# Performance work log

Measured on AMD Instinct MI355X. Metric: run time of the kernel, lower is better.

## Reference

```python
import jax, jax.numpy as jnp
import numpy as np

IN_DIM = 768
N_HEADS = 12
HEAD_DIM = IN_DIM // N_HEADS


def setup_inputs() -> dict:
    key = jax.random.key(0)
    k1, k2, k3, k4, k5 = jax.random.split(key, 5)
    x = jax.random.normal(k1, (2, 2048, IN_DIM), dtype=jnp.float32)
    s = 1.0 / np.sqrt(IN_DIM)
    W_qkv = jax.random.uniform(k2, (IN_DIM, 3 * IN_DIM), jnp.float32, -s, s)
    b_qkv = jax.random.uniform(k3, (3 * IN_DIM,), jnp.float32, -s, s)
    W_out = jax.random.uniform(k4, (IN_DIM, IN_DIM), jnp.float32, -s, s)
    b_out = jax.random.uniform(k5, (IN_DIM,), jnp.float32, -s, s)
    return {"x": x, "W_qkv": W_qkv, "b_qkv": b_qkv, "W_out": W_out, "b_out": b_out}


def reference(x, W_qkv, b_qkv, W_out, b_out):
    B, N, D = x.shape
    qkv = x @ W_qkv + b_qkv  # [B, N, 3D]
    qkv = qkv.reshape(B, N, 3, N_HEADS, HEAD_DIM)
    qkv = jnp.transpose(qkv, (2, 0, 3, 1, 4))  # [3, B, H, N, Dh]
    q, k, v = qkv[0], qkv[1], qkv[2]
    scale = 1.0 / np.sqrt(HEAD_DIM)
    scores = jnp.einsum("bhqd,bhkd->bhqk", q, k) * scale  # [B, H, N, N]
    attn = jax.nn.softmax(scores, axis=-1)
    out = jnp.einsum("bhqk,bhkd->bhqd", attn, v)  # [B, H, N, Dh]
    out = jnp.transpose(out, (0, 2, 1, 3)).reshape(B, N, D)
    return out @ W_out + b_out
```

## Files before the change

### kernel.cpp

```cpp
#include <hip/hip_runtime.h>

#define DEVI __device__ __forceinline__

typedef __attribute__((ext_vector_type(8))) short short8;
typedef __attribute__((ext_vector_type(4))) float f32x4;

DEVI unsigned short f32_to_bf16(float f) {
  unsigned int u = __float_as_uint(f);
  u += 0x7fffu + ((u >> 16) & 1u);
  return (unsigned short)(u >> 16);
}
DEVI float bf16_to_f32(unsigned short h) {
  return __uint_as_float(((unsigned int)h) << 16);
}

DEVI void gld_lds16(const void* g, void* l) {
  __builtin_amdgcn_global_load_lds(
      (__attribute__((address_space(1))) void*)(g),
      (__attribute__((address_space(3))) void*)(l), 16, 0, 0);
}

__global__ void k_cast_bf16(const float* __restrict__ in, unsigned short* __restrict__ out,
                            int total8) {
  int i = blockIdx.x * blockDim.x + threadIdx.x;
  if (i >= total8) return;
  const float* src = in + i * 8;
  short8 v;
#pragma unroll
  for (int j = 0; j < 8; ++j) v[j] = (short)f32_to_bf16(src[j]);
  *(short8*)&out[(size_t)i * 8] = v;
}

__global__ __launch_bounds__(256) void k_cast_Bt(const float* __restrict__ W,
                                                 unsigned short* __restrict__ Wt,
                                                 int K, int N) {
  int kt = blockIdx.x, nt = blockIdx.y;
  __shared__ float t[32][33];
  int tid = threadIdx.x;
#pragma unroll
  for (int p = 0; p < 4; ++p) {
    int idx = tid + p * 256;
    int rr = idx >> 5, cc = idx & 31;
    t[rr][cc] = W[(size_t)(kt * 32 + rr) * N + nt * 32 + cc];
  }
  __syncthreads();
#pragma unroll
  for (int p = 0; p < 4; ++p) {
    int idx = tid + p * 256;
    int rn = idx >> 5, ck = idx & 31;
    Wt[(size_t)(nt * 32 + rn) * K + kt * 32 + ck] = f32_to_bf16(t[ck][rn]);
  }
}

__global__ __launch_bounds__(256) void k_gemm_qkv(const unsigned short* __restrict__ A,
                                                  const unsigned short* __restrict__ Bt,
                                                  const float* __restrict__ bias,
                                                  int M, int N, int K,
                                                  unsigned short* __restrict__ Qo,
                                                  unsigned short* __restrict__ Ko,
                                                  unsigned short* __restrict__ Vo) {
  __shared__ __align__(16) unsigned short As[128 * 32];
  __shared__ __align__(16) unsigned short Bs[128 * 32];
  int tid = threadIdx.x;
  int tm = blockIdx.x, tn = blockIdx.y;
  int lane = tid & 63, wid = tid >> 6;
  int wr = wid >> 1, wc = wid & 1;
  int g = lane >> 4, lr = lane & 15;
  f32x4 acc[4][4] = {};
  int srow = tid >> 2;
  int scol = (tid & 3) * 8;
  const unsigned short* Ab = A + (size_t)tm * 128 * K;
  const unsigned short* Bb = Bt + (size_t)tn * 128 * K;
  for (int k0 = 0; k0 < K; k0 += 32) {
    gld_lds16(Ab + (size_t)srow * K + k0 + scol, &As[srow * 32 + scol]);
    gld_lds16(Ab + (size_t)(srow + 64) * K + k0 + scol, &As[(srow + 64) * 32 + scol]);
    gld_lds16(Bb + (size_t)srow * K + k0 + scol, &Bs[srow * 32 + scol]);
    gld_lds16(Bb + (size_t)(srow + 64) * K + k0 + scol, &Bs[(srow + 64) * 32 + scol]);
    __syncthreads();
    short8 a[4], b[4];
#pragma unroll
    for (int m = 0; m < 4; ++m)
      a[m] = *(const short8*)&As[(wr * 64 + m * 16 + lr) * 32 + g * 8];
#pragma unroll
    for (int n = 0; n < 4; ++n)
      b[n] = *(const short8*)&Bs[(wc * 64 + n * 16 + lr) * 32 + g * 8];
#pragma unroll
    for (int m = 0; m < 4; ++m)
#pragma unroll
      for (int n = 0; n < 4; ++n)
        acc[m][n] = __builtin_amdgcn_mfma_f32_16x16x32_bf16(a[m], b[n], acc[m][n], 0, 0, 0);
    __syncthreads();
  }
  const float QSCALE = 0.125f * 1.4426950408889634f;
#pragma unroll
  for (int m = 0; m < 4; ++m) {
#pragma unroll
    for (int n = 0; n < 4; ++n) {
      int col = tn * 128 + wc * 64 + n * 16 + lr;
      float bv = bias[col];
      int sec = (col >= 1536) ? 2 : ((col >= 768) ? 1 : 0);
      int c = col - sec * 768;
      int hh = c >> 6, d = c & 63;
#pragma unroll
      for (int j = 0; j < 4; ++j) {
        int row = tm * 128 + wr * 64 + m * 16 + g * 4 + j;
        int bb = row >> 11, nn = row & 2047;
        size_t dst = (((size_t)(bb * 12 + hh) << 11) + nn) * 64 + d;
        float outv = acc[m][n][j] + bv;
        if (sec == 0) {
          Qo[dst] = f32_to_bf16(outv * QSCALE);
        } else if (sec == 1) {
          Ko[dst] = f32_to_bf16(outv);
        } else {
          Vo[dst] = f32_to_bf16(outv);
        }
      }
    }
  }
}

__global__ __launch_bounds__(256) void k_gemm2(const unsigned short* __restrict__ A,
                                               const unsigned short* __restrict__ Bt,
                                               const float* __restrict__ bias,
                                               float* __restrict__ C,
                                               int M, int N, int K) {
  __shared__ __align__(16) unsigned short As[64 * 32];
  __shared__ __align__(16) unsigned short Bs[64 * 32];
  int tid = threadIdx.x;
  int tm = blockIdx.x, tn = blockIdx.y;
  int lane = tid & 63, wid = tid >> 6;
  int wr = wid >> 1, wc = wid & 1;
  int g = lane >> 4, lr = lane & 15;
  f32x4 acc[2][2] = {};
  int srow = tid >> 2;
  int scol = (tid & 3) * 8;
  const unsigned short* Ab = A + (size_t)tm * 64 * K;
  const unsigned short* Bb = Bt + (size_t)tn * 64 * K;
  for (int k0 = 0; k0 < K; k0 += 32) {
    gld_lds16(Ab + (size_t)srow * K + k0 + scol, &As[srow * 32 + scol]);
    gld_lds16(Bb + (size_t)srow * K + k0 + scol, &Bs[srow * 32 + scol]);
    __syncthreads();
    short8 a[2], b[2];
#pragma unroll
    for (int m = 0; m < 2; ++m)
      a[m] = *(const short8*)&As[(wr * 32 + m * 16 + lr) * 32 + g * 8];
#pragma unroll
    for (int n = 0; n < 2; ++n)
      b[n] = *(const short8*)&Bs[(wc * 32 + n * 16 + lr) * 32 + g * 8];
#pragma unroll
    for (int m = 0; m < 2; ++m)
#pragma unroll
      for (int n = 0; n < 2; ++n)
        acc[m][n] = __builtin_amdgcn_mfma_f32_16x16x32_bf16(a[m], b[n], acc[m][n], 0, 0, 0);
    __syncthreads();
  }
#pragma unroll
  for (int m = 0; m < 2; ++m) {
#pragma unroll
    for (int n = 0; n < 2; ++n) {
      int col = tn * 64 + wc * 32 + n * 16 + lr;
      float bv = bias[col];
#pragma unroll
      for (int j = 0; j < 4; ++j) {
        int row = tm * 64 + wr * 32 + m * 16 + g * 4 + j;
        C[(size_t)row * N + col] = acc[m][n][j] + bv;
      }
    }
  }
}

__global__ __launch_bounds__(256) void k_v_transpose(const unsigned short* __restrict__ Vc,
                                                     unsigned short* __restrict__ Vt) {
  int bh = blockIdx.x;
  int nt = blockIdx.y;
  __shared__ unsigned short s[64][65];
  int tid = threadIdx.x;
  int r = tid >> 2;
#pragma unroll
  for (int p = 0; p < 2; ++p) {
    int c = (tid & 3) + p * 4;
    short8 v = *(const short8*)&Vc[((size_t)(bh * 2048 + nt * 64 + r)) * 64 + c * 8];
#pragma unroll
    for (int ii = 0; ii < 8; ++ii) s[r][c * 8 + ii] = (unsigned short)v[ii];
  }
  __syncthreads();
  int d = tid >> 2;
#pragma unroll
  for (int p = 0; p < 2; ++p) {
    int c = (tid & 3) + p * 4;
    short8 w;
#pragma unroll
    for (int ii = 0; ii < 8; ++ii) w[ii] = (short)s[c * 8 + ii][d];
    *(short8*)&Vt[((size_t)bh * 64 + d) * 2048 + nt * 64 + c * 8] = w;
  }
}


#define ATTN_STAGE(KSB, VSB, T)                                                          \
  {                                                                                      \
    int kv0 = (T) * 64;                                                                  \
    _Pragma("unroll") for (int it = 0; it < 2; ++it) {                                   \
      int L = tid + it * 256;                                                            \
      int rw = L >> 3, s7 = L & 7;                                                       \
      gld_lds16(Kb + (size_t)(khead + kv0 + rw) * 64 + ((s7 ^ (rw & 7)) * 8),            \
                &KSB[L * 8]);                                                            \
      gld_lds16(Vt + (size_t)(vhead + rw) * 2048 + kv0 + ((s7 ^ (rw & 7)) * 8),          \
                &VSB[L * 8]);                                                            \
    }                                                                                    \
  }

#define PS_WRITE(M)                                                                      \
  {                                                                                      \
    unsigned int d0, d1;                                                                 \
    asm("v_cvt_pk_bf16_f32 %0, %1, %2" : "=v"(d0) : "v"(s[M][0]), "v"(s[M][1]));         \
    asm("v_cvt_pk_bf16_f32 %0, %1, %2" : "=v"(d1) : "v"(s[M][2]), "v"(s[M][3]));         \
    uint2 w;                                                                             \
    w.x = d0;                                                                            \
    w.y = d1;                                                                            \
    *(uint2*)&Ps[wid][lr * 64 + ((((M)*2 + (g >> 1)) ^ lr) & 7) * 8 + (g & 1) * 4] = w;  \
  }

#define PV_KK(KK, VSB)                                                                   \
  {                                                                                      \
    short8 pa = *(const short8*)&Ps[wid][lr * 64 + ((((KK)*4 + g) ^ lr) & 7) * 8];       \
    __builtin_amdgcn_s_setprio(1);                                                       \
    _Pragma("unroll") for (int nt = 0; nt < 4; ++nt) {                                   \
      short8 vb = *(const short8*)&VSB[(nt * 16 + lr) * 64 +                             \
                                       ((((KK)*4 + g) ^ (lr & 7)) & 7) * 8];             \
      oacc[nt] = __builtin_amdgcn_mfma_f32_16x16x32_bf16(pa, vb, oacc[nt], 0, 0, 0);     \
    }                                                                                    \
    __builtin_amdgcn_s_setprio(0);                                                       \
  }

#define PROC_TILE(KSB, VSB)                                                              \
  {                                                                                      \
    f32x4 s[4];                                                                          \
    __builtin_amdgcn_s_setprio(1);                                                       \
    _Pragma("unroll") for (int m = 0; m < 4; ++m) {                                      \
      short8 kf0 = *(const short8*)&KSB[(m * 16 + lr) * 64 + ((g ^ (lr & 7)) * 8)];      \
      short8 kf1 =                                                                       \
          *(const short8*)&KSB[(m * 16 + lr) * 64 + (((g + 4) ^ (lr & 7)) * 8)];         \
      f32x4 z = {0.f, 0.f, 0.f, 0.f};                                                    \
      z = __builtin_amdgcn_mfma_f32_16x16x32_bf16(kf0, qf0, z, 0, 0, 0);                 \
      s[m] = __builtin_amdgcn_mfma_f32_16x16x32_bf16(kf1, qf1, z, 0, 0, 0);              \
    }                                                                                    \
    __builtin_amdgcn_s_setprio(0);                                                       \
    _Pragma("unroll") for (int m = 0; m < 4; ++m) {                                      \
      _Pragma("unroll") for (int j = 0; j < 4; ++j) {                                    \
        float pv = exp2f(s[m][j]);                                                       \
        s[m][j] = pv;                                                                    \
        lrun += pv;                                                                      \
      }                                                                                  \
    }                                                                                    \
    PS_WRITE(0)                                                                          \
    PS_WRITE(1)                                                                          \
    PV_KK(0, VSB)                                                                        \
    PS_WRITE(2)                                                                          \
    PS_WRITE(3)                                                                          \
    PV_KK(1, VSB)                                                                        \
  }

__global__ __launch_bounds__(256, 4) void k_attn(const unsigned short* __restrict__ Qb,
                                                 const unsigned short* __restrict__ Kb,
                                                 const unsigned short* __restrict__ Vt,
                                                 unsigned short* __restrict__ Xh) {
  int bh = blockIdx.x;
  int qb = blockIdx.y;
  int b = bh / 12, h = bh - b * 12;
  __shared__ __align__(16) unsigned short Ks0[64 * 64], Ks1[64 * 64];
  __shared__ __align__(16) unsigned short Vs0[64 * 64], Vs1[64 * 64];
  __shared__ __align__(16) unsigned short Ps[4][16 * 64];
  int tid = threadIdx.x;
  int wid = tid >> 6, lane = tid & 63;
  int g = lane >> 4, lr = lane & 15;
  int khead = bh * 2048;
  int vhead = bh * 64;
  int q0 = qb * 64 + wid * 16;

  short8 qf0 = *(const short8*)&Qb[(size_t)(khead + q0 + lr) * 64 + g * 8];
  short8 qf1 = *(const short8*)&Qb[(size_t)(khead + q0 + lr) * 64 + 32 + g * 8];

  float lrun = 0.f;
  f32x4 oacc[4] = {};

  ATTN_STAGE(Ks0, Vs0, 0);
  __syncthreads();
#pragma unroll 1
  for (int tt = 0; tt < 16; ++tt) {
    ATTN_STAGE(Ks1, Vs1, 2 * tt + 1);
    PROC_TILE(Ks0, Vs0);
    __syncthreads();
    if (tt < 15) ATTN_STAGE(Ks0, Vs0, 2 * tt + 2);
    PROC_TILE(Ks1, Vs1);
    __syncthreads();
  }

  lrun += __shfl_xor(lrun, 16, 64);
  lrun += __shfl_xor(lrun, 32, 64);
  float linv = 1.0f / lrun;
  float lf[4];
#pragma unroll
  for (int j = 0; j < 4; ++j) lf[j] = __shfl(linv, g * 4 + j, 64);
#pragma unroll
  for (int nt = 0; nt < 4; ++nt)
#pragma unroll
    for (int j = 0; j < 4; ++j) {
      int row = b * 2048 + q0 + g * 4 + j;
      int col = h * 64 + nt * 16 + lr;
      Xh[(size_t)row * 768 + col] = f32_to_bf16(oacc[nt][j] * lf[j]);
    }
}

extern "C" void kernel_launch(void* const* d_in, const int* in_sizes, int n_in,
                              void* d_out, int out_size, void* d_ws, size_t ws_size,
                              hipStream_t stream) {
  const float* x = (const float*)d_in[0];
  const float* W_qkv = (const float*)d_in[1];
  const float* b_qkv = (const float*)d_in[2];
  const float* W_out = (const float*)d_in[3];
  const float* b_out = (const float*)d_in[4];
  float* out = (float*)d_out;
  char* ws = (char*)d_ws;

  unsigned short* Xh = (unsigned short*)(ws + 0);
  unsigned short* Xb = (unsigned short*)(ws + 18874368);
  unsigned short* Wq_t = (unsigned short*)(ws + 25165824);
  unsigned short* Wo_t = (unsigned short*)(ws + 28704768);
  unsigned short* Qb = (unsigned short*)(ws + 32243712);
  unsigned short* Kb = (unsigned short*)(ws + 38535168);
  unsigned short* Vc = (unsigned short*)(ws + 44826624);
  unsigned short* Vt = (unsigned short*)(ws + 51118080);

  k_cast_bf16<<<(4096 * 768 / 8 + 255) / 256, 256, 0, stream>>>(x, Xb, 4096 * 768 / 8);
  k_cast_Bt<<<dim3(24, 72), 256, 0, stream>>>(W_qkv, Wq_t, 768, 2304);
  k_cast_Bt<<<dim3(24, 24), 256, 0, stream>>>(W_out, Wo_t, 768, 768);
  k_gemm_qkv<<<dim3(32, 18), 256, 0, stream>>>(Xb, Wq_t, b_qkv, 4096, 2304, 768, Qb, Kb, Vc);
  k_v_transpose<<<dim3(24, 32), 256, 0, stream>>>(Vc, Vt);
  k_attn<<<dim3(24, 32), 256, 0, stream>>>(Qb, Kb, Vt, Xh);
  k_gemm2<<<dim3(64, 12), 256, 0, stream>>>(Xh, Wo_t, b_out, out, 4096, 768, 768);
}
```

Baseline: 110.9 us.

## Switch attention to 32x32x16 MFMA with register-resident P via permlane swap

The attention kernel now uses 2 waves of 32 query rows each instead of 4 waves of 16, with 32x32x16 bf16 MFMAs for both QK^T and PV. The P tile is converted to bf16 and rearranged into the A-operand layout in registers using v_permlane32_swap, which removes the LDS round-trip through the Ps buffer. This aims to cut LDS traffic and per-tile instruction overhead, but it raises register pressure (larger accumulators) and halves the threads per block for the same LDS staging.

```diff
diff --git a/kernel.cpp b/kernel.cpp
--- a/kernel.cpp
+++ b/kernel.cpp
@@ -4,6 +4,7 @@
 
 typedef __attribute__((ext_vector_type(8))) short short8;
 typedef __attribute__((ext_vector_type(4))) float f32x4;
+typedef __attribute__((ext_vector_type(16))) float f32x16;
 
 DEVI unsigned short f32_to_bf16(float f) {
   unsigned int u = __float_as_uint(f);
@@ -199,8 +200,8 @@
 #define ATTN_STAGE(KSB, VSB, T)                                                          \
   {                                                                                      \
     int kv0 = (T) * 64;                                                                  \
-    _Pragma("unroll") for (int it = 0; it < 2; ++it) {                                   \
-      int L = tid + it * 256;                                                            \
+    _Pragma("unroll") for (int it = 0; it < 4; ++it) {                                   \
+      int L = tid + it * 128;                                                            \
       int rw = L >> 3, s7 = L & 7;                                                       \
       gld_lds16(Kb + (size_t)(khead + kv0 + rw) * 64 + ((s7 ^ (rw & 7)) * 8),            \
                 &KSB[L * 8]);                                                            \
@@ -209,58 +210,69 @@
     }                                                                                    \
   }
 
-#define PS_WRITE(M)                                                                      \
+#define BUILD_PA(S, KS0)                                                                 \
   {                                                                                      \
-    unsigned int d0, d1;                                                                 \
-    asm("v_cvt_pk_bf16_f32 %0, %1, %2" : "=v"(d0) : "v"(s[M][0]), "v"(s[M][1]));         \
-    asm("v_cvt_pk_bf16_f32 %0, %1, %2" : "=v"(d1) : "v"(s[M][2]), "v"(s[M][3]));         \
-    uint2 w;                                                                             \
-    w.x = d0;                                                                            \
-    w.y = d1;                                                                            \
-    *(uint2*)&Ps[wid][lr * 64 + ((((M)*2 + (g >> 1)) ^ lr) & 7) * 8 + (g & 1) * 4] = w;  \
-  }
-
-#define PV_KK(KK, VSB)                                                                   \
-  {                                                                                      \
-    short8 pa = *(const short8*)&Ps[wid][lr * 64 + ((((KK)*4 + g) ^ lr) & 7) * 8];       \
-    __builtin_amdgcn_s_setprio(1);                                                       \
-    _Pragma("unroll") for (int nt = 0; nt < 4; ++nt) {                                   \
-      short8 vb = *(const short8*)&VSB[(nt * 16 + lr) * 64 +                             \
-                                       ((((KK)*4 + g) ^ (lr & 7)) & 7) * 8];             \
-      oacc[nt] = __builtin_amdgcn_mfma_f32_16x16x32_bf16(pa, vb, oacc[nt], 0, 0, 0);     \
-    }                                                                                    \
-    __builtin_amdgcn_s_setprio(0);                                                       \
+    unsigned int b0, a0, e0, c0;                                                         \
+    asm("v_cvt_pk_bf16_f32 %0, %1, %2" : "=v"(b0) : "v"(S[0]), "v"(S[1]));               \
+    asm("v_cvt_pk_bf16_f32 %0, %1, %2" : "=v"(a0) : "v"(S[4]), "v"(S[5]));               \
+    asm("v_permlane32_swap_b32 %0, %1" : "+v"(b0), "+v"(a0));                            \
+    asm("v_cvt_pk_bf16_f32 %0, %1, %2" : "=v"(e0) : "v"(S[2]), "v"(S[3]));               \
+    asm("v_cvt_pk_bf16_f32 %0, %1, %2" : "=v"(c0) : "v"(S[6]), "v"(S[7]));               \
+    asm("v_permlane32_swap_b32 %0, %1" : "+v"(e0), "+v"(c0));                            \
+    paw[KS0][0] = b0; paw[KS0][1] = e0; paw[KS0][2] = a0; paw[KS0][3] = c0;              \
+    unsigned int b1, a1, e1, c1;                                                         \
+    asm("v_cvt_pk_bf16_f32 %0, %1, %2" : "=v"(b1) : "v"(S[8]), "v"(S[9]));               \
+    asm("v_cvt_pk_bf16_f32 %0, %1, %2" : "=v"(a1) : "v"(S[12]), "v"(S[13]));             \
+    asm("v_permlane32_swap_b32 %0, %1" : "+v"(b1), "+v"(a1));                            \
+    asm("v_cvt_pk_bf16_f32 %0, %1, %2" : "=v"(e1) : "v"(S[10]), "v"(S[11]));             \
+    asm("v_cvt_pk_bf16_f32 %0, %1, %2" : "=v"(c1) : "v"(S[14]), "v"(S[15]));             \
+    asm("v_permlane32_swap_b32 %0, %1" : "+v"(e1), "+v"(c1));                            \
+    paw[KS0 + 1][0] = b1; paw[KS0 + 1][1] = e1; paw[KS0 + 1][2] = a1; paw[KS0 + 1][3] = c1; \
   }
 
 #define PROC_TILE(KSB, VSB)                                                              \
   {                                                                                      \
-    f32x4 s[4];                                                                          \
+    f32x16 sa = {}, sb = {};                                                             \
     __builtin_amdgcn_s_setprio(1);                                                       \
-    _Pragma("unroll") for (int m = 0; m < 4; ++m) {                                      \
-      short8 kf0 = *(const short8*)&KSB[(m * 16 + lr) * 64 + ((g ^ (lr & 7)) * 8)];      \
-      short8 kf1 =                                                                       \
-          *(const short8*)&KSB[(m * 16 + lr) * 64 + (((g + 4) ^ (lr & 7)) * 8)];         \
-      f32x4 z = {0.f, 0.f, 0.f, 0.f};                                                    \
-      z = __builtin_amdgcn_mfma_f32_16x16x32_bf16(kf0, qf0, z, 0, 0, 0);                 \
-      s[m] = __builtin_amdgcn_mfma_f32_16x16x32_bf16(kf1, qf1, z, 0, 0, 0);              \
+    _Pragma("unroll") for (int ds = 0; ds < 4; ++ds) {                                   \
+      short8 kf0 = *(const short8*)&KSB[ln31 * 64 + (((ds * 2 + hi) ^ ln7) * 8)];        \
+      short8 kf1 = *(const short8*)&KSB[(32 + ln31) * 64 + (((ds * 2 + hi) ^ ln7) * 8)]; \
+      sa = __builtin_amdgcn_mfma_f32_32x32x16_bf16(kf0, qf[ds], sa, 0, 0, 0);            \
+      sb = __builtin_amdgcn_mfma_f32_32x32x16_bf16(kf1, qf[ds], sb, 0, 0, 0);            \
     }                                                                                    \
     __builtin_amdgcn_s_setprio(0);                                                       \
-    _Pragma("unroll") for (int m = 0; m < 4; ++m) {                                      \
-      _Pragma("unroll") for (int j = 0; j < 4; ++j) {                                    \
-        float pv = exp2f(s[m][j]);                                                       \
-        s[m][j] = pv;                                                                    \
-        lrun += pv;                                                                      \
-      }                                                                                  \
-    }                                                                                    \
-    PS_WRITE(0)                                                                          \
-    PS_WRITE(1)                                                                          \
-    PV_KK(0, VSB)                                                                        \
-    PS_WRITE(2)                                                                          \
-    PS_WRITE(3)                                                                          \
-    PV_KK(1, VSB)                                                                        \
-  }
-
-__global__ __launch_bounds__(256, 4) void k_attn(const unsigned short* __restrict__ Qb,
+    _Pragma("unroll") for (int i = 0; i < 16; ++i) {                                     \
+      float pv = exp2f(sa[i]);                                                           \
+      sa[i] = pv;                                                                        \
+      lrun += pv;                                                                        \
+    }                                                                                    \
+    _Pragma("unroll") for (int i = 0; i < 16; ++i) {                                     \
+      float pv = exp2f(sb[i]);                                                           \
+      sb[i] = pv;                                                                        \
+      lrun += pv;                                                                        \
+    }                                                                                    \
+    unsigned int paw[4][4];                                                              \
+    BUILD_PA(sa, 0)                                                                      \
+    BUILD_PA(sb, 2)                                                                      \
+    __builtin_amdgcn_s_setprio(1);                                                       \
+    _Pragma("unroll") for (int ks = 0; ks < 4; ++ks) {                                   \
+      union {                                                                            \
+        unsigned int u[4];                                                               \
+        short8 s8;                                                                       \
+      } pu;                                                                              \
+      pu.u[0] = paw[ks][0];                                                              \
+      pu.u[1] = paw[ks][1];                                                              \
+      pu.u[2] = paw[ks][2];                                                              \
+      pu.u[3] = paw[ks][3];                                                              \
+      short8 vb0 = *(const short8*)&VSB[ln31 * 64 + (((ks * 2 + hi) ^ ln7) * 8)];        \
+      short8 vb1 = *(const short8*)&VSB[(32 + ln31) * 64 + (((ks * 2 + hi) ^ ln7) * 8)]; \
+      oacc0 = __builtin_amdgcn_mfma_f32_32x32x16_bf16(pu.s8, vb0, oacc0, 0, 0, 0);       \
+      oacc1 = __builtin_amdgcn_mfma_f32_32x32x16_bf16(pu.s8, vb1, oacc1, 0, 0, 0);       \
+    }                                                                                    \
+    __builtin_amdgcn_s_setprio(0);                                                       \
+  }
+
+__global__ __launch_bounds__(128, 3) void k_attn(const unsigned short* __restrict__ Qb,
                                                  const unsigned short* __restrict__ Kb,
                                                  const unsigned short* __restrict__ Vt,
                                                  unsigned short* __restrict__ Xh) {
@@ -269,19 +281,20 @@
   int b = bh / 12, h = bh - b * 12;
   __shared__ __align__(16) unsigned short Ks0[64 * 64], Ks1[64 * 64];
   __shared__ __align__(16) unsigned short Vs0[64 * 64], Vs1[64 * 64];
-  __shared__ __align__(16) unsigned short Ps[4][16 * 64];
   int tid = threadIdx.x;
   int wid = tid >> 6, lane = tid & 63;
-  int g = lane >> 4, lr = lane & 15;
+  int ln31 = lane & 31, hi = lane >> 5, ln7 = lane & 7;
   int khead = bh * 2048;
   int vhead = bh * 64;
-  int q0 = qb * 64 + wid * 16;
-
-  short8 qf0 = *(const short8*)&Qb[(size_t)(khead + q0 + lr) * 64 + g * 8];
-  short8 qf1 = *(const short8*)&Qb[(size_t)(khead + q0 + lr) * 64 + 32 + g * 8];
+  int q0 = qb * 64 + wid * 32;
+
+  short8 qf[4];
+#pragma unroll
+  for (int ds = 0; ds < 4; ++ds)
+    qf[ds] = *(const short8*)&Qb[(size_t)(khead + q0 + ln31) * 64 + ds * 16 + hi * 8];
 
   float lrun = 0.f;
-  f32x4 oacc[4] = {};
+  f32x16 oacc0 = {}, oacc1 = {};
 
   ATTN_STAGE(Ks0, Vs0, 0);
   __syncthreads();
@@ -295,20 +308,17 @@
     __syncthreads();
   }
 
-  lrun += __shfl_xor(lrun, 16, 64);
   lrun += __shfl_xor(lrun, 32, 64);
   float linv = 1.0f / lrun;
-  float lf[4];
-#pragma unroll
-  for (int j = 0; j < 4; ++j) lf[j] = __shfl(linv, g * 4 + j, 64);
-#pragma unroll
-  for (int nt = 0; nt < 4; ++nt)
-#pragma unroll
-    for (int j = 0; j < 4; ++j) {
-      int row = b * 2048 + q0 + g * 4 + j;
-      int col = h * 64 + nt * 16 + lr;
-      Xh[(size_t)row * 768 + col] = f32_to_bf16(oacc[nt][j] * lf[j]);
-    }
+#pragma unroll
+  for (int r = 0; r < 16; ++r) {
+    int qrow = (r & 3) + 8 * (r >> 2) + 4 * hi;
+    float lf = __shfl(linv, qrow, 64);
+    int grow = b * 2048 + q0 + qrow;
+    int colb = h * 64 + ln31;
+    Xh[(size_t)grow * 768 + colb] = f32_to_bf16(oacc0[r] * lf);
+    Xh[(size_t)grow * 768 + colb + 32] = f32_to_bf16(oacc1[r] * lf);
+  }
 }
 
 extern "C" void kernel_launch(void* const* d_in, const int* in_sizes, int n_in,
@@ -336,6 +346,6 @@
   k_cast_Bt<<<dim3(24, 24), 256, 0, stream>>>(W_out, Wo_t, 768, 768);
   k_gemm_qkv<<<dim3(32, 18), 256, 0, stream>>>(Xb, Wq_t, b_qkv, 4096, 2304, 768, Qb, Kb, Vc);
   k_v_transpose<<<dim3(24, 32), 256, 0, stream>>>(Vc, Vt);
-  k_attn<<<dim3(24, 32), 256, 0, stream>>>(Qb, Kb, Vt, Xh);
+  k_attn<<<dim3(24, 32), 128, 0, stream>>>(Qb, Kb, Vt, Xh);
   k_gemm2<<<dim3(64, 12), 256, 0, stream>>>(Xh, Wo_t, b_out, out, 4096, 768, 768);
 }
```

New measurement: 118.2 us. 6.6% more time.
